# Performance work log

Hardware: AMD Instinct MI355X
Metric: run time of the kernel (lower is better)

## Reference

```python
import jax, jax.numpy as jnp
import numpy as np

N_USERS = 100000
N_ITEMS = 50000
D = 64
N_LAYERS = 3
E_RAW = 2_000_000
B = 4096


def setup_inputs() -> dict:
    rng = np.random.RandomState(0)
    u = rng.randint(0, N_USERS, E_RAW).astype(np.int64)
    i = rng.randint(0, N_ITEMS, E_RAW).astype(np.int64)
    lin = np.unique(u * N_ITEMS + i)  # dedupe interactions like the dok_matrix would
    u = (lin // N_ITEMS).astype(np.int32)
    i = (lin % N_ITEMS).astype(np.int32)
    deg_u = np.bincount(u, minlength=N_USERS).astype(np.float64)
    deg_i = np.bincount(i, minlength=N_ITEMS).astype(np.float64)
    inv_u = np.where(deg_u > 0, 1.0 / np.sqrt(np.maximum(deg_u, 1.0)), 0.0)
    inv_i = np.where(deg_i > 0, 1.0 / np.sqrt(np.maximum(deg_i, 1.0)), 0.0)
    val = (inv_u[u] * inv_i[i]).astype(np.float32)  # D^-1/2 A D^-1/2 entries
    # symmetric bipartite Laplacian: user block rows then item block rows
    rows = np.concatenate([u, i + N_USERS]).astype(np.int32)
    cols = np.concatenate([i + N_USERS, u]).astype(np.int32)
    vals = np.concatenate([val, val])

    key = jax.random.key(0)
    k1, k2, k3, k4 = jax.random.split(key, 4)
    embeds = jax.random.normal(k1, (N_USERS + N_ITEMS, D), jnp.float32) * 0.1
    users = jax.random.randint(k2, (B,), 0, N_USERS)
    pos_items = jax.random.randint(k3, (B,), 0, N_ITEMS)
    neg_items = jax.random.randint(k4, (B,), 0, N_ITEMS)
    return dict(embeds=embeds, vals=jnp.asarray(vals), rows=jnp.asarray(rows),
                cols=jnp.asarray(cols), users=users, pos_items=pos_items,
                neg_items=neg_items)


def reference(embeds, vals, rows, cols, users, pos_items, neg_items):
    N = N_USERS + N_ITEMS
    cur = embeds
    acc = embeds  # running sum over layer embeddings (incl. layer 0)
    for _ in range(N_LAYERS):
        msg = vals[:, None] * cur[cols]                      # [nnz, D] gather
        cur = jax.ops.segment_sum(msg, rows, num_segments=N)  # SpMM scatter-add
        acc = acc + cur
    mean = acc / (N_LAYERS + 1)
    user_e = mean[:N_USERS]
    item_e = mean[N_USERS:]
    return user_e[users], item_e[pos_items], item_e[neg_items]
```

## Files before the change

### kernel.cpp

```cpp
#include <hip/hip_runtime.h>
#include <hip/hip_bf16.h>

#define N_USERS 100000
#define N_ITEMS 50000
#define N_TOT   150000
#define D       64
#define BSHIFT  6
#define NBUCK   ((N_ITEMS + 63) >> 6)
#define BCAP    3072
#define CONVU_B 391
#define FLAG_B  48
#define SCAT_K  16

typedef float v2f __attribute__((ext_vector_type(2)));

__device__ __forceinline__ unsigned bf16rn(float f) {
    unsigned x = __float_as_uint(f);
    return (x + 0x7FFFu + ((x >> 16) & 1u)) >> 16;
}
__device__ __forceinline__ unsigned packbf(float a, float b) {
    return bf16rn(a) | (bf16rn(b) << 16);
}
__device__ __forceinline__ int lower_bound(const int* __restrict__ a, int n, int key) {
    int lo = 0, hi = n;
    while (lo < hi) {
        int mid = (lo + hi) >> 1;
        if (a[mid] < key) lo = mid + 1; else hi = mid;
    }
    return lo;
}

__global__ __launch_bounds__(256) void pre1_kernel(
        const float* __restrict__ embeds, const int* __restrict__ rows,
        int* __restrict__ user_ptr, unsigned* __restrict__ ebfS,
        float* __restrict__ invrow,
        const int* __restrict__ users, const int* __restrict__ pos,
        const int* __restrict__ neg, unsigned char* __restrict__ flags,
        int E, int B) {
    int b = blockIdx.x, t = threadIdx.x;
    if (b < CONVU_B) {
        __shared__ int ptr_s[257];
        __shared__ float inv_s[256];
        int base = b * 256;
        int r = base + t;
        int v = lower_bound(rows, E, r);
        ptr_s[t] = v;
        if (r <= N_USERS) user_ptr[r] = v;
        if (t == 0) ptr_s[256] = lower_bound(rows, E, base + 256);
        __syncthreads();
        if (r < N_USERS) {
            int deg = ptr_s[t + 1] - ptr_s[t];
            float inv = (deg > 0) ? (float)(1.0 / sqrt((double)deg)) : 0.f;
            inv_s[t] = inv;
            invrow[r] = inv;
        } else inv_s[t] = 0.f;
        __syncthreads();
        int fl = t & 15;
        #pragma unroll
        for (int i = 0; i < 16; ++i) {
            int lr = i * 16 + (t >> 4);
            int row = base + lr;
            if (row < N_USERS) {
                float inv = inv_s[lr];
                float4 v4 = *(const float4*)(embeds + (size_t)row * D + fl * 4);
                uint2 o;
                o.x = packbf(inv * v4.x, inv * v4.y);
                o.y = packbf(inv * v4.z, inv * v4.w);
                *(uint2*)(ebfS + (size_t)row * 32 + fl * 2) = o;
            }
        }
    } else {
        int k = (b - CONVU_B) * 256 + t;
        if (k < 3 * B) {
            int row;
            if (k < B)          row = users[k];
            else if (k < 2 * B) row = N_USERS + pos[k - B];
            else                row = N_USERS + neg[k - 2 * B];
            flags[row] = 1;
        }
    }
}

__global__ __launch_bounds__(256) void pre2_kernel(
        const int* __restrict__ rows, const int* __restrict__ cols,
        int* __restrict__ ccur, int* __restrict__ tmp,
        unsigned short* __restrict__ cols16, int E) {
    int b = blockIdx.x, t = threadIdx.x;
    __shared__ int ebuf[256 * SCAT_K];
    __shared__ unsigned short bbuf[256 * SCAT_K];
    __shared__ int cnt[NBUCK];
    __shared__ int basep[NBUCK];
    int chunk = b * (256 * SCAT_K);
    for (int i = t; i < NBUCK; i += 256) cnt[i] = 0;
    __syncthreads();
    #pragma unroll 8
    for (int k = 0; k < SCAT_K; ++k) {
        int e = chunk + k * 256 + t;
        int idx = k * 256 + t;
        if (e < E) {
            int i = cols[e] - N_USERS;
            cols16[e] = (unsigned short)i;
            int bu = i >> BSHIFT;
            ebuf[idx] = ((i & 63) << 17) | rows[e];
            bbuf[idx] = (unsigned short)bu;
            atomicAdd(&cnt[bu], 1);
        } else bbuf[idx] = 0xFFFFu;
    }
    __syncthreads();
    for (int i = t; i < NBUCK; i += 256) {
        int c = cnt[i];
        basep[i] = c ? atomicAdd(&ccur[i], c) : 0;
        cnt[i] = 0;
    }
    __syncthreads();
    #pragma unroll 4
    for (int k = 0; k < SCAT_K; ++k) {
        int idx = k * 256 + t;
        int bu = bbuf[idx];
        if (bu < NBUCK) {
            int pos2 = basep[bu] + atomicAdd(&cnt[bu], 1);
            if (pos2 < BCAP)
                tmp[(size_t)bu * BCAP + pos2] = ebuf[idx];
        }
    }
}

__global__ __launch_bounds__(256) void preB_kernel(
        const int* __restrict__ tmp, const int* __restrict__ ccur,
        const float* __restrict__ embeds,
        int* __restrict__ item_beg, int* __restrict__ item_end,
        int* __restrict__ nbr, unsigned* __restrict__ ebfS,
        unsigned* __restrict__ bb1, float* __restrict__ invrow) {
    int b = blockIdx.x, t = threadIdx.x;
    if (b == NBUCK) {
        if (t < 16) {
            *(uint2*)(ebfS + (size_t)N_TOT * 32 + t * 2) = make_uint2(0u, 0u);
            *(uint2*)(bb1  + (size_t)N_TOT * 32 + t * 2) = make_uint2(0u, 0u);
        }
        if (t == 0) invrow[N_TOT] = 0.f;
        return;
    }
    __shared__ int hist[64];
    __shared__ int scn[64];
    __shared__ int curs[64];
    __shared__ float inv_s[64];
    int n = ccur[b]; if (n > BCAP) n = BCAP;
    const int* src = tmp + (size_t)b * BCAP;
    if (t < 64) hist[t] = 0;
    __syncthreads();
    int n4 = n >> 2;
    const int4* src4 = (const int4*)src;
    for (int p = t; p < n4; p += 256) {
        int4 q = src4[p];
        atomicAdd(&hist[q.x >> 17], 1);
        atomicAdd(&hist[q.y >> 17], 1);
        atomicAdd(&hist[q.z >> 17], 1);
        atomicAdd(&hist[q.w >> 17], 1);
    }
    for (int p = (n4 << 2) + t; p < n; p += 256)
        atomicAdd(&hist[src[p] >> 17], 1);
    __syncthreads();
    if (t < 64) scn[t] = hist[t];
    __syncthreads();
    for (int off = 1; off < 64; off <<= 1) {
        int x = (t >= off && t < 64) ? scn[t - off] : 0;
        __syncthreads();
        if (t < 64) scn[t] += x;
        __syncthreads();
    }
    if (t < 64) {
        int excl = scn[t] - hist[t];
        curs[t] = excl;
        int gi = (b << BSHIFT) + t;
        float inv = (hist[t] > 0) ? (float)(1.0 / sqrt((double)hist[t])) : 0.f;
        inv_s[t] = inv;
        if (gi < N_ITEMS) {
            item_beg[gi] = b * BCAP + excl;
            item_end[gi] = b * BCAP + excl + hist[t];
            invrow[N_USERS + gi] = inv;
        }
    }
    __syncthreads();
    int* dst = nbr + (size_t)b * BCAP;
    for (int p = t; p < n4; p += 256) {
        int4 q = src4[p];
        int p0 = atomicAdd(&curs[q.x >> 17], 1); dst[p0] = q.x & 0x1FFFF;
        int p1 = atomicAdd(&curs[q.y >> 17], 1); dst[p1] = q.y & 0x1FFFF;
        int p2 = atomicAdd(&curs[q.z >> 17], 1); dst[p2] = q.z & 0x1FFFF;
        int p3 = atomicAdd(&curs[q.w >> 17], 1); dst[p3] = q.w & 0x1FFFF;
    }
    for (int p = (n4 << 2) + t; p < n; p += 256) {
        int q = src[p];
        int pos = atomicAdd(&curs[q >> 17], 1);
        dst[pos] = q & 0x1FFFF;
    }
    int fl = t & 15;
    #pragma unroll
    for (int i = 0; i < 4; ++i) {
        int lr = i * 16 + (t >> 4);
        int gi = (b << BSHIFT) + lr;
        if (gi < N_ITEMS) {
            int row = N_USERS + gi;
            float inv = inv_s[lr];
            float4 v4 = *(const float4*)(embeds + (size_t)row * D + fl * 4);
            uint2 o;
            o.x = packbf(inv * v4.x, inv * v4.y);
            o.y = packbf(inv * v4.z, inv * v4.w);
            *(uint2*)(ebfS + (size_t)row * 32 + fl * 2) = o;
        }
    }
}

__global__ __launch_bounds__(256) void agg_kernel(
        const unsigned* __restrict__ gsrc,
        float* __restrict__ nxt, unsigned* __restrict__ nxtb,
        const float* __restrict__ invrow,
        const unsigned char* __restrict__ flags,
        const int* __restrict__ user_ptr, const unsigned short* __restrict__ cols16,
        const int* __restrict__ item_beg, const int* __restrict__ item_end,
        const int* __restrict__ nbr) {
    int wave = (int)((blockIdx.x * blockDim.x + threadIdx.x) >> 6);
    int lane = (int)(threadIdx.x & 63);
    if (wave >= N_TOT) return;
    int g  = lane >> 3;
    int fl = lane & 7;

    bool is_user = wave < N_USERS;
    int s, epos, dummy;
    const unsigned* sb;
    if (is_user) {
        s = user_ptr[wave]; epos = user_ptr[wave + 1];
        sb = gsrc + (size_t)N_USERS * 32; dummy = N_ITEMS;
    } else {
        int i = wave - N_USERS; s = item_beg[i]; epos = item_end[i];
        sb = gsrc; dummy = N_TOT;
    }

    v2f a0 = {0.f, 0.f}, a1 = {0.f, 0.f}, a2 = {0.f, 0.f}, a3 = {0.f, 0.f};

    for (int base = s; base < epos; base += 64) {
        int cnt = epos - base; if (cnt > 64) cnt = 64;
        int col = dummy;
        if (lane < cnt)
            col = is_user ? (int)cols16[base + lane] : nbr[base + lane];
        int tcount = (cnt + 7) >> 3;
        #pragma unroll 8
        for (int t = 0; t < tcount; ++t) {
            int c = __shfl(col, 8 * t + g);
            uint4 q = *(const uint4*)(sb + (size_t)c * 32 + fl * 4);
            v2f p0 = {__uint_as_float(q.x << 16), __uint_as_float(q.x & 0xFFFF0000u)};
            v2f p1 = {__uint_as_float(q.y << 16), __uint_as_float(q.y & 0xFFFF0000u)};
            v2f p2 = {__uint_as_float(q.z << 16), __uint_as_float(q.z & 0xFFFF0000u)};
            v2f p3 = {__uint_as_float(q.w << 16), __uint_as_float(q.w & 0xFFFF0000u)};
            a0 += p0; a1 += p1; a2 += p2; a3 += p3;
        }
    }
    float acc[8] = {a0.x, a0.y, a1.x, a1.y, a2.x, a2.y, a3.x, a3.y};
    #pragma unroll
    for (int j = 0; j < 8; ++j) {
        acc[j] += __shfl_xor(acc[j], 8);
        acc[j] += __shfl_xor(acc[j], 16);
        acc[j] += __shfl_xor(acc[j], 32);
    }
    if (lane < 8) {
        float inv = invrow[wave];
        float f[8];
        #pragma unroll
        for (int j = 0; j < 8; ++j) f[j] = inv * acc[j];
        uint4 o;
        o.x = packbf(inv * f[0], inv * f[1]); o.y = packbf(inv * f[2], inv * f[3]);
        o.z = packbf(inv * f[4], inv * f[5]); o.w = packbf(inv * f[6], inv * f[7]);
        *(uint4*)(nxtb + (size_t)wave * 32 + fl * 4) = o;
        if (flags[wave]) {
            size_t ro = (size_t)wave * D + fl * 8;
            *(float4*)(nxt + ro)     = make_float4(f[0], f[1], f[2], f[3]);
            *(float4*)(nxt + ro + 4) = make_float4(f[4], f[5], f[6], f[7]);
        }
    }
}

__global__ __launch_bounds__(256) void agg3_fused_kernel(
        const unsigned* __restrict__ gsrc,
        const float* __restrict__ e0, const float* __restrict__ e1,
        const float* __restrict__ e2, const float* __restrict__ invrow,
        const int* __restrict__ users, const int* __restrict__ pos,
        const int* __restrict__ neg,
        const int* __restrict__ user_ptr, const unsigned short* __restrict__ cols16,
        const int* __restrict__ item_beg, const int* __restrict__ item_end,
        const int* __restrict__ nbr,
        float* __restrict__ out, int B) {
    int slot = (int)((blockIdx.x * blockDim.x + threadIdx.x) >> 6);
    int lane = (int)(threadIdx.x & 63);
    if (slot >= 3 * B) return;
    int g  = lane >> 3;
    int fl = lane & 7;

    int row;
    if (slot < B)          row = users[slot];
    else if (slot < 2 * B) row = N_USERS + pos[slot - B];
    else                   row = N_USERS + neg[slot - 2 * B];

    bool is_user = row < N_USERS;
    int s, epos, dummy;
    const unsigned* sb;
    if (is_user) {
        s = user_ptr[row]; epos = user_ptr[row + 1];
        sb = gsrc + (size_t)N_USERS * 32; dummy = N_ITEMS;
    } else {
        int i = row - N_USERS; s = item_beg[i]; epos = item_end[i];
        sb = gsrc; dummy = N_TOT;
    }

    v2f a0 = {0.f, 0.f}, a1 = {0.f, 0.f}, a2 = {0.f, 0.f}, a3 = {0.f, 0.f};

    for (int base = s; base < epos; base += 64) {
        int cnt = epos - base; if (cnt > 64) cnt = 64;
        int col = dummy;
        if (lane < cnt)
            col = is_user ? (int)cols16[base + lane] : nbr[base + lane];
        int tcount = (cnt + 7) >> 3;
        #pragma unroll 8
        for (int t = 0; t < tcount; ++t) {
            int c = __shfl(col, 8 * t + g);
            uint4 q = *(const uint4*)(sb + (size_t)c * 32 + fl * 4);
            v2f p0 = {__uint_as_float(q.x << 16), __uint_as_float(q.x & 0xFFFF0000u)};
            v2f p1 = {__uint_as_float(q.y << 16), __uint_as_float(q.y & 0xFFFF0000u)};
            v2f p2 = {__uint_as_float(q.z << 16), __uint_as_float(q.z & 0xFFFF0000u)};
            v2f p3 = {__uint_as_float(q.w << 16), __uint_as_float(q.w & 0xFFFF0000u)};
            a0 += p0; a1 += p1; a2 += p2; a3 += p3;
        }
    }
    float acc[8] = {a0.x, a0.y, a1.x, a1.y, a2.x, a2.y, a3.x, a3.y};
    #pragma unroll
    for (int j = 0; j < 8; ++j) {
        acc[j] += __shfl_xor(acc[j], 8);
        acc[j] += __shfl_xor(acc[j], 16);
        acc[j] += __shfl_xor(acc[j], 32);
    }
    if (lane < 8) {
        float inv = invrow[row];
        size_t ro = (size_t)row * D + fl * 8;
        float4 x0 = *(const float4*)(e0 + ro), x1 = *(const float4*)(e0 + ro + 4);
        float4 y0 = *(const float4*)(e1 + ro), y1 = *(const float4*)(e1 + ro + 4);
        float4 z0 = *(const float4*)(e2 + ro), z1 = *(const float4*)(e2 + ro + 4);
        float4 r0, r1;
        r0.x = (x0.x + y0.x + z0.x + inv * acc[0]) * 0.25f;
        r0.y = (x0.y + y0.y + z0.y + inv * acc[1]) * 0.25f;
        r0.z = (x0.z + y0.z + z0.z + inv * acc[2]) * 0.25f;
        r0.w = (x0.w + y0.w + z0.w + inv * acc[3]) * 0.25f;
        r1.x = (x1.x + y1.x + z1.x + inv * acc[4]) * 0.25f;
        r1.y = (x1.y + y1.y + z1.y + inv * acc[5]) * 0.25f;
        r1.z = (x1.z + y1.z + z1.z + inv * acc[6]) * 0.25f;
        r1.w = (x1.w + y1.w + z1.w + inv * acc[7]) * 0.25f;
        size_t oo = (size_t)slot * D + fl * 8;
        *(float4*)(out + oo)     = r0;
        *(float4*)(out + oo + 4) = r1;
    }
}

extern "C" void kernel_launch(void* const* d_in, const int* in_sizes, int n_in,
                              void* d_out, int out_size, void* d_ws, size_t ws_size,
                              hipStream_t stream) {
    const float* embeds = (const float*)d_in[0];
    const int*   rows   = (const int*)d_in[2];
    const int*   cols   = (const int*)d_in[3];
    const int*   users  = (const int*)d_in[4];
    const int*   pos    = (const int*)d_in[5];
    const int*   neg    = (const int*)d_in[6];
    const int E2 = in_sizes[1];
    const int E  = E2 / 2;
    const int B  = in_sizes[4];

    char* ws = (char*)d_ws;
    size_t off = 0;
    auto alloc = [&](size_t bytes) { void* p = ws + off; off = (off + bytes + 255) & ~(size_t)255; return p; };
    float*    buf1     = (float*)   alloc((size_t)N_TOT * D * sizeof(float));
    float*    buf2     = (float*)   alloc((size_t)N_TOT * D * sizeof(float));
    unsigned* ebfS     = (unsigned*)alloc((size_t)(N_TOT + 1) * 32 * sizeof(unsigned));
    unsigned* bb1      = (unsigned*)alloc((size_t)(N_TOT + 1) * 32 * sizeof(unsigned));
    int*      nbr      = (int*)     alloc((size_t)NBUCK * BCAP * sizeof(int));
    unsigned short* cols16 = (unsigned short*)alloc((size_t)E * sizeof(unsigned short));
    int*      user_ptr = (int*)     alloc((size_t)(N_USERS + 1) * sizeof(int));
    int*      item_beg = (int*)     alloc((size_t)N_ITEMS * sizeof(int));
    int*      item_end = (int*)     alloc((size_t)N_ITEMS * sizeof(int));
    float*    invrow   = (float*)   alloc((size_t)(N_TOT + 1) * sizeof(float));
    int*      ccur     = (int*)     alloc((size_t)NBUCK * sizeof(int));
    unsigned char* flags = (unsigned char*)alloc((size_t)N_TOT);
    int*      tmp      = (int*)buf1;

    size_t zspan = ((char*)flags + N_TOT) - (char*)ccur;
    hipMemsetAsync(ccur, 0, zspan, stream);
    pre1_kernel<<<CONVU_B + FLAG_B, 256, 0, stream>>>(
        embeds, rows, user_ptr, ebfS, invrow, users, pos, neg, flags, E, B);
    const int scatB = (E + 256 * SCAT_K - 1) / (256 * SCAT_K);
    pre2_kernel<<<scatB, 256, 0, stream>>>(rows, cols, ccur, tmp, cols16, E);
    preB_kernel<<<NBUCK + 1, 256, 0, stream>>>(
        tmp, ccur, embeds, item_beg, item_end, nbr, ebfS, bb1, invrow);

    const int blocks = (N_TOT + 3) / 4;
    agg_kernel<<<blocks, 256, 0, stream>>>(ebfS, buf1, bb1, invrow, flags, user_ptr,
                                           cols16, item_beg, item_end, nbr);
    agg_kernel<<<blocks, 256, 0, stream>>>(bb1, buf2, ebfS, invrow, flags, user_ptr,
                                           cols16, item_beg, item_end, nbr);

    agg3_fused_kernel<<<(3 * B + 3) / 4, 256, 0, stream>>>(
        ebfS, embeds, buf1, buf2, invrow, users, pos, neg,
        user_ptr, cols16, item_beg, item_end, nbr, (float*)d_out, B);
}
```

Measured before the change: 334.5 us.

## Pad per-block bucket reservations to 16 and re-read cols instead of LDS staging

The bucket scatter kernel no longer stages edges in shared memory. It re-reads cols/rows from global memory in a second pass, and each block's bucket reservation is rounded up to a multiple of 16 and the gap filled with a sentinel. This frees LDS, so each block can handle three times as many edges (SCAT_K 48), and the padding keeps each block's writes aligned. The histogram/sort kernel skips sentinel entries. The cost is a larger BCAP buffer, extra global reads, sentinel writes, and a risk of overflowing buckets when padding accumulates.

Measured after the change: 365.4 us. 1.09x slower.

```diff
diff --git a/kernel.cpp b/kernel.cpp
--- a/kernel.cpp
+++ b/kernel.cpp
@@ -7,10 +7,11 @@
 #define D       64
 #define BSHIFT  6
 #define NBUCK   ((N_ITEMS + 63) >> 6)
-#define BCAP    3072
+#define BCAP    4608
 #define CONVU_B 391
 #define FLAG_B  48
-#define SCAT_K  16
+#define SCAT_K  48
+#define SENT    (64 << 17)
 
 typedef float v2f __attribute__((ext_vector_type(2)));
 
@@ -86,8 +87,6 @@
         int* __restrict__ ccur, int* __restrict__ tmp,
         unsigned short* __restrict__ cols16, int E) {
     int b = blockIdx.x, t = threadIdx.x;
-    __shared__ int ebuf[256 * SCAT_K];
-    __shared__ unsigned short bbuf[256 * SCAT_K];
     __shared__ int cnt[NBUCK];
     __shared__ int basep[NBUCK];
     int chunk = b * (256 * SCAT_K);
@@ -96,31 +95,45 @@
     #pragma unroll 8
     for (int k = 0; k < SCAT_K; ++k) {
         int e = chunk + k * 256 + t;
-        int idx = k * 256 + t;
         if (e < E) {
             int i = cols[e] - N_USERS;
             cols16[e] = (unsigned short)i;
-            int bu = i >> BSHIFT;
-            ebuf[idx] = ((i & 63) << 17) | rows[e];
-            bbuf[idx] = (unsigned short)bu;
-            atomicAdd(&cnt[bu], 1);
-        } else bbuf[idx] = 0xFFFFu;
+            atomicAdd(&cnt[i >> BSHIFT], 1);
+        }
     }
     __syncthreads();
     for (int i = t; i < NBUCK; i += 256) {
         int c = cnt[i];
-        basep[i] = c ? atomicAdd(&ccur[i], c) : 0;
+        int res = (c + 15) & ~15;
+        int bp = 0;
+        if (res) {
+            bp = atomicAdd(&ccur[i], res);
+            if (bp + res > BCAP) bp = BCAP;
+        }
+        basep[i] = bp;
         cnt[i] = 0;
     }
     __syncthreads();
     #pragma unroll 4
     for (int k = 0; k < SCAT_K; ++k) {
-        int idx = k * 256 + t;
-        int bu = bbuf[idx];
-        if (bu < NBUCK) {
-            int pos2 = basep[bu] + atomicAdd(&cnt[bu], 1);
-            if (pos2 < BCAP)
-                tmp[(size_t)bu * BCAP + pos2] = ebuf[idx];
+        int e = chunk + k * 256 + t;
+        if (e < E) {
+            int i = cols[e] - N_USERS;
+            int bu = i >> BSHIFT;
+            int p = atomicAdd(&cnt[bu], 1);
+            int gp = basep[bu] + p;
+            if (gp < BCAP)
+                tmp[(size_t)bu * BCAP + gp] = ((i & 63) << 17) | rows[e];
+        }
+    }
+    __syncthreads();
+    for (int i = t; i < NBUCK; i += 256) {
+        int c = cnt[i];
+        int res = (c + 15) & ~15;
+        int bp = basep[i];
+        for (int p = c; p < res; ++p) {
+            int gp = bp + p;
+            if (gp < BCAP) tmp[(size_t)i * BCAP + gp] = SENT;
         }
     }
 }
@@ -152,13 +165,15 @@
     const int4* src4 = (const int4*)src;
     for (int p = t; p < n4; p += 256) {
         int4 q = src4[p];
-        atomicAdd(&hist[q.x >> 17], 1);
-        atomicAdd(&hist[q.y >> 17], 1);
-        atomicAdd(&hist[q.z >> 17], 1);
-        atomicAdd(&hist[q.w >> 17], 1);
-    }
-    for (int p = (n4 << 2) + t; p < n; p += 256)
-        atomicAdd(&hist[src[p] >> 17], 1);
+        if (q.x < SENT) atomicAdd(&hist[q.x >> 17], 1);
+        if (q.y < SENT) atomicAdd(&hist[q.y >> 17], 1);
+        if (q.z < SENT) atomicAdd(&hist[q.z >> 17], 1);
+        if (q.w < SENT) atomicAdd(&hist[q.w >> 17], 1);
+    }
+    for (int p = (n4 << 2) + t; p < n; p += 256) {
+        int q = src[p];
+        if (q < SENT) atomicAdd(&hist[q >> 17], 1);
+    }
     __syncthreads();
     if (t < 64) scn[t] = hist[t];
     __syncthreads();
@@ -184,15 +199,14 @@
     int* dst = nbr + (size_t)b * BCAP;
     for (int p = t; p < n4; p += 256) {
         int4 q = src4[p];
-        int p0 = atomicAdd(&curs[q.x >> 17], 1); dst[p0] = q.x & 0x1FFFF;
-        int p1 = atomicAdd(&curs[q.y >> 17], 1); dst[p1] = q.y & 0x1FFFF;
-        int p2 = atomicAdd(&curs[q.z >> 17], 1); dst[p2] = q.z & 0x1FFFF;
-        int p3 = atomicAdd(&curs[q.w >> 17], 1); dst[p3] = q.w & 0x1FFFF;
+        if (q.x < SENT) { int p0 = atomicAdd(&curs[q.x >> 17], 1); dst[p0] = q.x & 0x1FFFF; }
+        if (q.y < SENT) { int p1 = atomicAdd(&curs[q.y >> 17], 1); dst[p1] = q.y & 0x1FFFF; }
+        if (q.z < SENT) { int p2 = atomicAdd(&curs[q.z >> 17], 1); dst[p2] = q.z & 0x1FFFF; }
+        if (q.w < SENT) { int p3 = atomicAdd(&curs[q.w >> 17], 1); dst[p3] = q.w & 0x1FFFF; }
     }
     for (int p = (n4 << 2) + t; p < n; p += 256) {
         int q = src[p];
-        int pos = atomicAdd(&curs[q >> 17], 1);
-        dst[pos] = q & 0x1FFFF;
+        if (q < SENT) { int pos = atomicAdd(&curs[q >> 17], 1); dst[pos] = q & 0x1FFFF; }
     }
     int fl = t & 15;
     #pragma unroll
```
